# Kernel optimization log

Measured on AMD Instinct MI355X. Metric: run time of the kernel, lower is better.

The kernel has to match this reference:

```python
import jax, jax.numpy as jnp
import numpy as np

B, T, C, H = 4, 2048, 1024, 16
D = C // H  # head_dim = 64


def setup_inputs() -> dict:
    key = jax.random.key(0)
    ks = jax.random.split(key, 4)
    scale = 1.0 / np.sqrt(C)
    return {
        "x": jax.random.normal(ks[0], (B, T, C), dtype=jnp.float32),
        "attn_mask": jnp.ones((B, T), dtype=jnp.int32),
        "W_qkv": jax.random.normal(ks[1], (C, 3 * C), dtype=jnp.float32) * scale,
        "b_qkv": jnp.zeros((3 * C,), dtype=jnp.float32),
        "W_proj": jax.random.normal(ks[2], (C, C), dtype=jnp.float32) * scale,
        "b_proj": jnp.zeros((C,), dtype=jnp.float32),
    }


def reference(x, attn_mask, W_qkv, b_qkv, W_proj, b_proj):
    b, t, c = x.shape
    qkv = x @ W_qkv + b_qkv                      # (B,T,3C)
    q, k, v = jnp.split(qkv, 3, axis=-1)
    # b t (h d) -> b h t d
    q = q.reshape(b, t, H, D).transpose(0, 2, 1, 3)
    k = k.reshape(b, t, H, D).transpose(0, 2, 1, 3)
    v = v.reshape(b, t, H, D).transpose(0, 2, 1, 3)
    att = jnp.einsum("bhtd,bhsd->bhts", q, k) / jnp.sqrt(jnp.float32(D))
    causal = jnp.tril(jnp.ones((t, t), dtype=bool))[None, None]       # (1,1,T,T)
    pad = (attn_mask[:, None, None, :t] != 0)                         # (B,1,1,T)
    att = jnp.where(causal & pad, att, -jnp.inf)
    att = jax.nn.softmax(att, axis=-1)
    y = jnp.einsum("bhts,bhsd->bhtd", att, v)   # (B,H,T,D)
    y = y.transpose(0, 2, 1, 3).reshape(b, t, c)
    return y @ W_proj + b_proj
```

## Files before the change

### kernel.cpp

```cpp
#include <hip/hip_runtime.h>
#include <math.h>

#define B_ 4
#define T_ 2048
#define C_ 1024
#define H_ 16
#define D_ 64
#define M_ (B_*T_)
#define N1_ (3*C_)

typedef __attribute__((ext_vector_type(8))) short bf16x8;
typedef __attribute__((ext_vector_type(4))) short bf16x4;
typedef __attribute__((ext_vector_type(4))) float f32x4;
typedef __attribute__((ext_vector_type(16))) float f32x16;

__device__ __forceinline__ short f2bf(float f){
  union { float f; unsigned u; } v; v.f = f;
  unsigned r = (v.u + 0x7fffu + ((v.u >> 16) & 1u)) >> 16;
  return (short)r;
}

__device__ __forceinline__ unsigned cvtpk(float lo, float hi){
  unsigned r;
  asm("v_cvt_pk_bf16_f32 %0, %1, %2" : "=v"(r) : "v"(lo), "v"(hi));
  return r;
}

__device__ __forceinline__ void plswap(unsigned &a, unsigned &b){
  asm volatile("v_permlane32_swap_b32 %0, %1" : "+v"(a), "+v"(b));
}
__device__ __forceinline__ float xhalf_add(float x){
  unsigned a = __float_as_uint(x), b = a;
  asm volatile("v_permlane32_swap_b32 %0, %1" : "+v"(a), "+v"(b));
  return __uint_as_float(a) + __uint_as_float(b);
}

__device__ __forceinline__ void gll16(const void* g, void* l){
  __builtin_amdgcn_global_load_lds((const __attribute__((address_space(1))) void*)g,
                                   (__attribute__((address_space(3))) void*)l, 16, 0, 0);
}

__global__ __launch_bounds__(256) void convx(const float* __restrict__ x, short* __restrict__ xb, int n){
  int i = (blockIdx.x*256 + threadIdx.x)*8;
  if (i >= n) return;
  float4 a = *(const float4*)(x+i), b = *(const float4*)(x+i+4);
  bf16x8 o;
  o[0]=f2bf(a.x); o[1]=f2bf(a.y); o[2]=f2bf(a.z); o[3]=f2bf(a.w);
  o[4]=f2bf(b.x); o[5]=f2bf(b.y); o[6]=f2bf(b.z); o[7]=f2bf(b.w);
  *(bf16x8*)(xb+i) = o;
}

__global__ __launch_bounds__(256) void transw(const float* __restrict__ W, short* __restrict__ Wt, int K, int N){
  __shared__ float tl[64][72];
  int tid = threadIdx.x;
  int n0 = blockIdx.x*64, k0 = blockIdx.y*64;
  #pragma unroll
  for (int i=0;i<4;i++){
    int row = (tid>>4) + i*16;
    int col4 = (tid&15)*4;
    float4 v = *(const float4*)&W[(size_t)(k0+row)*N + n0 + col4];
    *(float4*)&tl[row][col4] = v;
  }
  __syncthreads();
  #pragma unroll
  for (int i=0;i<2;i++){
    int nr = (tid>>3) + i*32;
    int ch = tid&7;
    bf16x8 o;
    #pragma unroll
    for (int e=0;e<8;e++) o[e] = f2bf(tl[ch*8+e][nr]);
    *(bf16x8*)&Wt[(size_t)(n0+nr)*K + k0 + ch*8] = o;
  }
}

template<int OUTBF>
__global__ __launch_bounds__(512) void gemm_bt(const short* __restrict__ A, const short* __restrict__ Bt,
           const float* __restrict__ bias, short* __restrict__ outb, float* __restrict__ outf,
           int M, int N, int K)
{
  __shared__ __attribute__((aligned(128))) char LDSC[147456];
  const int tid = threadIdx.x;
  const int wv = tid>>6, ln = tid&63;
  const int lnr = ln&15, lg = ln>>4;
  const int wm = wv>>1, wn = wv&1;
  const int nx = gridDim.x;
  const int nwg = nx*gridDim.y;
  const int lin = blockIdx.x + nx*blockIdx.y;
  const int swz = (lin&7)*(nwg>>3) + (lin>>3);
  const int m0 = (swz/nx)*256, n0 = (swz%nx)*128;

  const int srA = tid>>3;
  const int sg  = (tid&7) ^ (srA&7);
  const short* Ag = A  + (size_t)(m0 + srA)*K + sg*8;
  const short* Bg = Bt + (size_t)(n0 + srA)*K + sg*8;

  const int fsw = (lg ^ (lnr&7))<<4;
  const int aln = (wm*64 + lnr)*128 + fsw;
  const int bln = (wn*64 + lnr)*128 + fsw;

  auto STAGE = [&](int kt, int bi){
    const short* a = Ag + kt*64;
    const short* b = Bg + kt*64;
    char* ab = LDSC + bi*32768 + wv*1024;
    char* bb = LDSC + 98304 + bi*16384 + wv*1024;
    gll16(a,                ab);
    gll16(a + (size_t)64*K, ab + 8192);
    gll16(a + (size_t)128*K, ab + 16384);
    gll16(a + (size_t)192*K, ab + 24576);
    gll16(b,                bb);
    gll16(b + (size_t)64*K, bb + 8192);
  };

  f32x4 acc[4][4];
  #pragma unroll
  for (int i=0;i<4;i++)
    #pragma unroll
    for (int j=0;j<4;j++) acc[i][j] = (f32x4){0.f,0.f,0.f,0.f};

  const int NT = K >> 6;
  STAGE(0, 0);
  STAGE(1, 1);
  asm volatile("s_waitcnt vmcnt(6)" ::: "memory");
  __builtin_amdgcn_sched_barrier(0);
  __builtin_amdgcn_s_barrier();
  __builtin_amdgcn_sched_barrier(0);

  int cb = 0, sb = 2;
  #pragma unroll 1
  for (int kt = 0; kt < NT; kt++){
    if (kt + 2 < NT) STAGE(kt + 2, sb);

    const char* ab = LDSC + cb*32768;
    const char* bb = LDSC + 98304 + cb*16384;
    bf16x8 af[4][2], bfr[4][2];
    #pragma unroll
    for (int mi=0;mi<4;mi++)
      #pragma unroll
      for (int ks=0;ks<2;ks++)
        af[mi][ks] = *(const bf16x8*)(ab + ((aln + mi*2048) ^ (ks<<6)));
    #pragma unroll
    for (int ni=0;ni<4;ni++)
      #pragma unroll
      for (int ks=0;ks<2;ks++)
        bfr[ni][ks] = *(const bf16x8*)(bb + ((bln + ni*2048) ^ (ks<<6)));

    __builtin_amdgcn_s_setprio(1);
    #pragma unroll
    for (int mi=0;mi<4;mi++)
      #pragma unroll
      for (int ni=0;ni<4;ni++)
        #pragma unroll
        for (int ks=0;ks<2;ks++)
          acc[mi][ni] = __builtin_amdgcn_mfma_f32_16x16x32_bf16(af[mi][ks], bfr[ni][ks], acc[mi][ni], 0,0,0);
    __builtin_amdgcn_s_setprio(0);

    if (kt < NT-1){
      __builtin_amdgcn_sched_barrier(0);
      if (kt < NT-2){ asm volatile("s_waitcnt vmcnt(6)" ::: "memory"); }
      else          { asm volatile("s_waitcnt vmcnt(0)" ::: "memory"); }
      __builtin_amdgcn_sched_barrier(0);
      __builtin_amdgcn_s_barrier();
      __builtin_amdgcn_sched_barrier(0);
    }
    cb = (cb==2) ? 0 : cb+1;
    sb = (sb==2) ? 0 : sb+1;
  }

  #pragma unroll
  for (int mi=0;mi<4;mi++){
    #pragma unroll
    for (int ni=0;ni<4;ni++){
      int col = n0 + wn*64 + ni*16 + lnr;
      float bv = bias[col];
      #pragma unroll
      for (int r=0;r<4;r++){
        int row = m0 + wm*64 + mi*16 + lg*4 + r;
        float v = acc[mi][ni][r] + bv;
        if (OUTBF){
          if (col < C_) v *= 0.18033688f;
          outb[(size_t)row*N + col] = f2bf(v);
        } else {
          outf[(size_t)row*N + col] = v;
        }
      }
    }
  }
}

__global__ __launch_bounds__(256) void transv(const short* __restrict__ qkv, short* __restrict__ vt){
  __shared__ short tl[64][72];
  int tid = threadIdx.x;
  int t0 = blockIdx.x*64, bh = blockIdx.y;
  int b = bh>>4, h = bh&15;
  int tr = tid>>2, cc = (tid&3)*16;
  const short* src = &qkv[(size_t)(b*T_ + t0 + tr)*N1_ + 2*C_ + h*D_ + cc];
  #pragma unroll
  for (int i=0;i<4;i++){
    bf16x4 v = *(const bf16x4*)(src + i*4);
    *(bf16x4*)&tl[tr][cc + i*4] = v;
  }
  __syncthreads();
  int d = tid>>2, tc = (tid&3)*16;
  #pragma unroll
  for (int i=0;i<2;i++){
    bf16x8 o;
    #pragma unroll
    for (int e=0;e<8;e++) o[e] = tl[tc + i*8 + e][d];
    *(bf16x8*)&vt[(size_t)(bh*D_ + d)*T_ + t0 + tc + i*8] = o;
  }
}

__global__ __launch_bounds__(256) void attn14(const short* __restrict__ qkv, const short* __restrict__ vt,
           const int* __restrict__ mask, short* __restrict__ yb)
{
  __shared__ short Ks[64*64];
  __shared__ short Vs[64*64];
  const int tid = threadIdx.x;
  const int wv = tid>>6, ln = tid&63;
  const int l31 = ln & 31, hi = ln >> 5;
  const int bh = blockIdx.x, b = bh>>4, hd = bh&15;
  const int c = 15 - (int)blockIdx.y;
  const float MC = 11.541561f;

  const int srow = tid>>3;
  const int scol = (tid&7) ^ (srow&7);
  const short* kgb = qkv + (size_t)(b*T_ + srow)*N1_ + C_ + hd*D_ + scol*8;
  const short* vgb = vt  + (size_t)((bh<<6) + srow)*T_ + scol*8;
  int fa[4];
  #pragma unroll
  for (int i=0;i<4;i++)
    fa[i] = l31*128 + ((((i<<1)+hi) ^ (l31&7)) << 4);

  char* ksb = (char*)Ks;
  char* vsb = (char*)Vs;

  const int q0w = c*128 + wv*32;
  const int ntb  = 2*c + 2;
  const int myNt = 2*c + 1 + (wv>>1);

  bf16x8 qf[4];
  const short* qbase = qkv + (size_t)(b*T_ + q0w + l31)*N1_ + hd*D_ + hi*8;
  #pragma unroll
  for (int ds=0; ds<4; ds++) qf[ds] = *(const bf16x8*)(qbase + ds*16);

  f32x16 o0, o1;
  #pragma unroll
  for (int r=0;r<16;r++){ o0[r]=0.f; o1[r]=0.f; }
  float lsum = 0.f;

  #pragma unroll 1
  for (int jt = 0; jt < ntb; jt++){
    const int j0 = jt << 6;

    int mval = mask[b*T_ + j0 + ln];
    const short* kg = kgb + (size_t)j0*N1_;
    const short* vg = vgb + j0;
    gll16(kg,                    ksb + wv*1024);
    gll16(kg + (size_t)32*N1_,   ksb + 4096 + wv*1024);
    gll16(vg,                    vsb + wv*1024);
    gll16(vg + (size_t)32*T_,    vsb + 4096 + wv*1024);
    unsigned long long bm = __ballot(mval != 0);
    __syncthreads();

    if (jt < myNt){
      f32x16 s0, s1;
      #pragma unroll
      for (int r=0;r<16;r++){ s0[r]=-MC; s1[r]=-MC; }
      __builtin_amdgcn_s_setprio(1);
      #pragma unroll
      for (int ds=0; ds<4; ds++){
        bf16x8 k0 = *(const bf16x8*)(ksb + fa[ds]);
        bf16x8 k1 = *(const bf16x8*)(ksb + fa[ds] + 4096);
        s0 = __builtin_amdgcn_mfma_f32_32x32x16_bf16(k0, qf[ds], s0, 0,0,0);
        s1 = __builtin_amdgcn_mfma_f32_32x32x16_bf16(k1, qf[ds], s1, 0,0,0);
      }
      __builtin_amdgcn_s_setprio(0);

      const int qglob = q0w + l31;
      const bool allm = (bm == ~0ull);
      if (!allm){
        #pragma unroll
        for (int r=0;r<16;r++){
          int kr = (r&3) + 8*(r>>2) + 4*hi;
          bool ok0 = (j0 + kr      <= qglob) && ((bm >> kr) & 1);
          bool ok1 = (j0 + kr + 32 <= qglob) && ((bm >> (kr+32)) & 1);
          s0[r] = ok0 ? s0[r] : -INFINITY;
          s1[r] = ok1 ? s1[r] : -INFINITY;
        }
      } else if (j0 + 63 > q0w){
        #pragma unroll
        for (int r=0;r<16;r++){
          int kr = (r&3) + 8*(r>>2) + 4*hi;
          s0[r] = (j0 + kr      <= qglob) ? s0[r] : -INFINITY;
          s1[r] = (j0 + kr + 32 <= qglob) ? s1[r] : -INFINITY;
        }
      }

      #pragma unroll
      for (int r=0;r<16;r++){
        s0[r] = __builtin_amdgcn_exp2f(s0[r]);
        s1[r] = __builtin_amdgcn_exp2f(s1[r]);
      }
      float u[8];
      #pragma unroll
      for (int i=0;i<8;i++) u[i] = (s0[i]+s0[i+8]) + (s1[i]+s1[i+8]);
      #pragma unroll
      for (int i=0;i<4;i++) u[i] = u[i] + u[i+4];
      float ps = (u[0]+u[1]) + (u[2]+u[3]);
      lsum += xhalf_add(ps);

      unsigned LA[2][4], LB[2][4];
      #pragma unroll
      for (int rq=0; rq<4; rq++){
        LA[0][rq] = cvtpk(s0[4*rq],   s0[4*rq+1]);
        LB[0][rq] = cvtpk(s0[4*rq+2], s0[4*rq+3]);
        LA[1][rq] = cvtpk(s1[4*rq],   s1[4*rq+1]);
        LB[1][rq] = cvtpk(s1[4*rq+2], s1[4*rq+3]);
      }

      #pragma unroll
      for (int kt2=0; kt2<4; kt2++){
        const int kt = kt2>>1, sub = kt2&1;
        bf16x8 v0 = *(const bf16x8*)(vsb + fa[kt2]);
        bf16x8 v1 = *(const bf16x8*)(vsb + fa[kt2] + 4096);
        unsigned a0 = LA[kt][2*sub], a1 = LA[kt][2*sub+1];
        unsigned b0 = LB[kt][2*sub], b1 = LB[kt][2*sub+1];
        plswap(a0, a1);
        plswap(b0, b1);
        union { unsigned u[4]; bf16x8 v; } pf;
        pf.u[0] = a0; pf.u[1] = b0; pf.u[2] = a1; pf.u[3] = b1;
        __builtin_amdgcn_s_setprio(1);
        o0 = __builtin_amdgcn_mfma_f32_32x32x16_bf16(pf.v, v0, o0, 0,0,0);
        o1 = __builtin_amdgcn_mfma_f32_32x32x16_bf16(pf.v, v1, o1, 0,0,0);
        __builtin_amdgcn_s_setprio(0);
      }
    }
    __syncthreads();
  }

  float linv = 1.0f / lsum;
  #pragma unroll
  for (int r=0;r<16;r++){
    int qs = (r&3) + 8*(r>>2) + 4*hi;
    float lv = __shfl(linv, qs);
    size_t base = (size_t)(b*T_ + q0w + qs)*C_ + hd*D_ + l31;
    yb[base]      = f2bf(o0[r]*lv);
    yb[base + 32] = f2bf(o1[r]*lv);
  }
}

extern "C" void kernel_launch(void* const* d_in, const int* in_sizes, int n_in,
                              void* d_out, int out_size, void* d_ws, size_t ws_size,
                              hipStream_t stream){
  const float* x     = (const float*)d_in[0];
  const int*   mask  = (const int*)d_in[1];
  const float* Wqkv  = (const float*)d_in[2];
  const float* bqkv  = (const float*)d_in[3];
  const float* Wproj = (const float*)d_in[4];
  const float* bproj = (const float*)d_in[5];
  float* out = (float*)d_out;

  char* w = (char*)d_ws;
  short* xb     = (short*)w; w += (size_t)M_*C_*2;
  short* wqkvT  = (short*)w; w += (size_t)N1_*C_*2;
  short* wprojT = (short*)w; w += (size_t)C_*C_*2;
  short* qkvb   = (short*)w; w += (size_t)M_*N1_*2;
  short* vtb    = (short*)w; w += (size_t)B_*H_*D_*T_*2;
  short* yb     = (short*)w; w += (size_t)M_*C_*2;

  convx<<<dim3((M_*C_)/(256*8)), 256, 0, stream>>>(x, xb, M_*C_);
  transw<<<dim3(N1_/64, C_/64), 256, 0, stream>>>(Wqkv, wqkvT, C_, N1_);
  transw<<<dim3(C_/64,  C_/64), 256, 0, stream>>>(Wproj, wprojT, C_, C_);
  gemm_bt<1><<<dim3(N1_/128, M_/256), 512, 0, stream>>>(xb, wqkvT, bqkv, qkvb, nullptr, M_, N1_, C_);
  transv<<<dim3(T_/64, B_*H_), 256, 0, stream>>>(qkvb, vtb);
  attn14<<<dim3(B_*H_, 16), 256, 0, stream>>>(qkvb, vtb, mask, yb);
  gemm_bt<0><<<dim3(C_/128, M_/256), 512, 0, stream>>>(yb, wprojT, bproj, nullptr, out, M_, C_, C_);
}
```

Measured before the change: 179.5 us.

## Use 256x256 tile double-buffered GEMM for QKV projection

```diff
diff --git a/kernel.cpp b/kernel.cpp
--- a/kernel.cpp
+++ b/kernel.cpp
@@ -73,10 +73,107 @@
   }
 }
 
-template<int OUTBF>
-__global__ __launch_bounds__(512) void gemm_bt(const short* __restrict__ A, const short* __restrict__ Bt,
-           const float* __restrict__ bias, short* __restrict__ outb, float* __restrict__ outf,
-           int M, int N, int K)
+__global__ __launch_bounds__(512) void gemm256(const short* __restrict__ A, const short* __restrict__ Bt,
+           const float* __restrict__ bias, short* __restrict__ outb, int M, int N, int K)
+{
+  __shared__ __attribute__((aligned(128))) char LDSC[131072];
+  const int tid = threadIdx.x;
+  const int wv = tid>>6, ln = tid&63;
+  const int lnr = ln&15, lg = ln>>4;
+  const int wm = wv>>2, wn = wv&3;
+  const int nx = gridDim.x;
+  const int nwg = nx*gridDim.y;
+  const int lin = blockIdx.x + nx*blockIdx.y;
+  const int swz = (lin&7)*(nwg>>3) + (lin>>3);
+  const int m0 = (swz/nx)*256, n0 = (swz%nx)*256;
+
+  const int sr = tid>>3;
+  const int sg = (tid&7) ^ (sr&7);
+  const short* Ag = A  + (size_t)(m0 + sr)*K + sg*8;
+  const short* Bg = Bt + (size_t)(n0 + sr)*K + sg*8;
+  const int wv8 = wv*1024;
+
+  const int fsw = (lg ^ (lnr&7))<<4;
+  const int aln = (wm*128 + lnr)*128 + fsw;
+  const int bln = (wn*64  + lnr)*128 + fsw;
+
+  auto STAGE = [&](int kt, int bi){
+    const short* a = Ag + kt*64;
+    const short* b = Bg + kt*64;
+    char* ab = LDSC + bi*32768 + wv8;
+    char* bb = LDSC + 65536 + bi*32768 + wv8;
+    gll16(a,                 ab);
+    gll16(a + (size_t)64*K,  ab + 8192);
+    gll16(a + (size_t)128*K, ab + 16384);
+    gll16(a + (size_t)192*K, ab + 24576);
+    gll16(b,                 bb);
+    gll16(b + (size_t)64*K,  bb + 8192);
+    gll16(b + (size_t)128*K, bb + 16384);
+    gll16(b + (size_t)192*K, bb + 24576);
+  };
+
+  f32x4 acc[8][4];
+  #pragma unroll
+  for (int i=0;i<8;i++)
+    #pragma unroll
+    for (int j=0;j<4;j++) acc[i][j] = (f32x4){0.f,0.f,0.f,0.f};
+
+  const int NT = K >> 6;
+  STAGE(0, 0);
+  asm volatile("s_waitcnt vmcnt(0)" ::: "memory");
+  __builtin_amdgcn_sched_barrier(0);
+  __builtin_amdgcn_s_barrier();
+  __builtin_amdgcn_sched_barrier(0);
+
+  #pragma unroll 1
+  for (int kt = 0; kt < NT; kt++){
+    const int cb = kt & 1;
+    if (kt + 1 < NT) STAGE(kt + 1, cb ^ 1);
+
+    const char* ab = LDSC + cb*32768;
+    const char* bb = LDSC + 65536 + cb*32768;
+    #pragma unroll
+    for (int ks=0; ks<2; ks++){
+      bf16x8 af[8], bfr[4];
+      #pragma unroll
+      for (int mi=0;mi<8;mi++) af[mi]  = *(const bf16x8*)(ab + ((aln + mi*2048) ^ (ks<<6)));
+      #pragma unroll
+      for (int ni=0;ni<4;ni++) bfr[ni] = *(const bf16x8*)(bb + ((bln + ni*2048) ^ (ks<<6)));
+      __builtin_amdgcn_s_setprio(1);
+      #pragma unroll
+      for (int mi=0;mi<8;mi++)
+        #pragma unroll
+        for (int ni=0;ni<4;ni++)
+          acc[mi][ni] = __builtin_amdgcn_mfma_f32_16x16x32_bf16(af[mi], bfr[ni], acc[mi][ni], 0,0,0);
+      __builtin_amdgcn_s_setprio(0);
+    }
+
+    __builtin_amdgcn_sched_barrier(0);
+    asm volatile("s_waitcnt vmcnt(0)" ::: "memory");
+    __builtin_amdgcn_sched_barrier(0);
+    __builtin_amdgcn_s_barrier();
+    __builtin_amdgcn_sched_barrier(0);
+  }
+
+  #pragma unroll
+  for (int mi=0;mi<8;mi++){
+    #pragma unroll
+    for (int ni=0;ni<4;ni++){
+      int col = n0 + wn*64 + ni*16 + lnr;
+      float bv = bias[col];
+      #pragma unroll
+      for (int r=0;r<4;r++){
+        int row = m0 + wm*128 + mi*16 + lg*4 + r;
+        float v = acc[mi][ni][r] + bv;
+        if (col < C_) v *= 0.18033688f;
+        outb[(size_t)row*N + col] = f2bf(v);
+      }
+    }
+  }
+}
+
+__global__ __launch_bounds__(512) void gemm_proj(const short* __restrict__ A, const short* __restrict__ Bt,
+           const float* __restrict__ bias, float* __restrict__ outf, int M, int N, int K)
 {
   __shared__ __attribute__((aligned(128))) char LDSC[147456];
   const int tid = threadIdx.x;
@@ -175,13 +272,7 @@
       #pragma unroll
       for (int r=0;r<4;r++){
         int row = m0 + wm*64 + mi*16 + lg*4 + r;
-        float v = acc[mi][ni][r] + bv;
-        if (OUTBF){
-          if (col < C_) v *= 0.18033688f;
-          outb[(size_t)row*N + col] = f2bf(v);
-        } else {
-          outf[(size_t)row*N + col] = v;
-        }
+        outf[(size_t)row*N + col] = acc[mi][ni][r] + bv;
       }
     }
   }
@@ -371,8 +462,8 @@
   convx<<<dim3((M_*C_)/(256*8)), 256, 0, stream>>>(x, xb, M_*C_);
   transw<<<dim3(N1_/64, C_/64), 256, 0, stream>>>(Wqkv, wqkvT, C_, N1_);
   transw<<<dim3(C_/64,  C_/64), 256, 0, stream>>>(Wproj, wprojT, C_, C_);
-  gemm_bt<1><<<dim3(N1_/128, M_/256), 512, 0, stream>>>(xb, wqkvT, bqkv, qkvb, nullptr, M_, N1_, C_);
+  gemm256<<<dim3(N1_/256, M_/256), 512, 0, stream>>>(xb, wqkvT, bqkv, qkvb, M_, N1_, C_);
   transv<<<dim3(T_/64, B_*H_), 256, 0, stream>>>(qkvb, vtb);
   attn14<<<dim3(B_*H_, 16), 256, 0, stream>>>(qkvb, vtb, mask, yb);
-  gemm_bt<0><<<dim3(C_/128, M_/256), 512, 0, stream>>>(yb, wprojT, bproj, nullptr, out, M_, C_, C_);
-}
+  gemm_proj<<<dim3(C_/128, M_/256), 512, 0, stream>>>(yb, wprojT, bproj, out, M_, C_, C_);
+}
```

Result: faster. 170.4 us (-5.1%).
